# Optimization experiments

Measured on AMD Instinct MI355X. Metric: run time of the kernel, lower is better.

The kernel has to match this reference:

```python
import jax, jax.numpy as jnp
import numpy as np

B, S, D, H = 4, 2048, 1024, 16
DH = D // H


def setup_inputs() -> dict:
    key = jax.random.key(0)
    k1, k2, k3, k4, k5 = jax.random.split(key, 5)
    x = jax.random.normal(k1, (B, S, D), dtype=jnp.float32)
    mask = jnp.tril(jnp.ones((S, S), dtype=bool))  # causal mask
    scale = 1.0 / np.sqrt(D)
    w_qkv = jax.random.normal(k2, (D, 3 * D), dtype=jnp.float32) * scale
    b_qkv = jnp.zeros((3 * D,), dtype=jnp.float32)
    w_out = jax.random.normal(k3, (D, D), dtype=jnp.float32) * scale
    b_out = jnp.zeros((D,), dtype=jnp.float32)
    return {"x": x, "w_qkv": w_qkv, "b_qkv": b_qkv, "w_out": w_out, "b_out": b_out, "mask": mask}


def reference(x, w_qkv, b_qkv, w_out, b_out, mask):
    qkv = jnp.einsum('bsd,de->bse', x, w_qkv) + b_qkv  # (B,S,3D)
    q, k, v = jnp.split(qkv, 3, axis=-1)
    # (B,S,D) -> (B,H,S,DH)
    q = q.reshape(B, S, H, DH).transpose(0, 2, 1, 3)
    k = k.reshape(B, S, H, DH).transpose(0, 2, 1, 3)
    v = v.reshape(B, S, H, DH).transpose(0, 2, 1, 3)
    scores = jnp.einsum('bhqd,bhkd->bhqk', q, k) / jnp.sqrt(jnp.float32(DH))
    scores = jnp.where(mask[None, None, :, :], scores, -jnp.inf)
    attn = jax.nn.softmax(scores, axis=-1)  # dropout p=0.0 -> identity
    out = jnp.einsum('bhqk,bhkd->bhqd', attn, v)
    out = out.transpose(0, 2, 1, 3).reshape(B, S, D)
    return jnp.einsum('bsd,de->bse', out, w_out) + b_out
```

## Files before the change

### kernel.cpp

```cpp
#include <hip/hip_runtime.h>
#include <hip/hip_bf16.h>

typedef unsigned short u16;
typedef __bf16 bf16x8 __attribute__((ext_vector_type(8)));
typedef float f32x4 __attribute__((ext_vector_type(4)));
typedef unsigned short u16x8 __attribute__((ext_vector_type(8)));

__device__ __forceinline__ void async_copy16(void* lds, const void* g) {
  __builtin_amdgcn_global_load_lds(
      (const __attribute__((address_space(1))) unsigned int*)g,
      (__attribute__((address_space(3))) unsigned int*)lds, 16, 0, 0);
}

__device__ __forceinline__ u16 f2bf(float f) {
  __hip_bfloat16 h = __float2bfloat16(f);
  u16 u;
  __builtin_memcpy(&u, &h, 2);
  return u;
}

__device__ __forceinline__ u16 f2bf_rne(float f) {
  unsigned b = __builtin_bit_cast(unsigned, f);
  b += 0x7FFF + ((b >> 16) & 1);
  return (u16)(b >> 16);
}

__device__ __forceinline__ unsigned cvt_pk_bf16(float a, float b) {
  unsigned r;
  asm("v_cvt_pk_bf16_f32 %0, %1, %2" : "=v"(r) : "v"(a), "v"(b));
  return r;
}

__global__ void k_f32_to_bf16(const float* __restrict__ in, u16* __restrict__ out, int n4) {
  int i = blockIdx.x * blockDim.x + threadIdx.x;
  if (i >= n4) return;
  float4 v = ((const float4*)in)[i];
  ushort4 o;
  o.x = f2bf(v.x); o.y = f2bf(v.y); o.z = f2bf(v.z); o.w = f2bf(v.w);
  ((ushort4*)out)[i] = o;
}

__global__ void k_transpose_bf16(const float* __restrict__ in, u16* __restrict__ out, int R, int C) {
  __shared__ float tile[32][33];
  int bx = blockIdx.x * 32;
  int by = blockIdx.y * 32;
  int tx = threadIdx.x & 31, ty = threadIdx.x >> 5;
  for (int i = ty; i < 32; i += 8) tile[i][tx] = in[(size_t)(by + i) * C + bx + tx];
  __syncthreads();
  for (int i = ty; i < 32; i += 8) out[(size_t)(bx + i) * R + by + tx] = f2bf(tile[tx][i]);
}

template <int OUT_BF16>
__global__ __launch_bounds__(256, 2) void k_gemm_bt(
    const u16* __restrict__ A, const u16* __restrict__ Bt,
    const float* __restrict__ bias, void* __restrict__ Cout,
    int M, int N, int K) {
  __shared__ __align__(16) u16 As[128][32];
  __shared__ __align__(16) u16 Bs[128][32];
  const int t = threadIdx.x;
  const int l = t & 63, w = t >> 6;
  const int lr = l & 15, lk = l >> 4;
  const int wr = w >> 1, wc = w & 1;
  const int m0 = blockIdx.x * 128, n0 = blockIdx.y * 128;

  f32x4 acc[4][4] = {};

  for (int k0 = 0; k0 < K; k0 += 32) {
    __syncthreads();
    for (int c = 0; c < 2; ++c) {
      int idx = c * 256 + t;
      int row = idx >> 2, slot = idx & 3;
      int sw = (slot ^ ((row >> 1) & 3)) << 3;
      async_copy16((char*)&As[0][0] + idx * 16, A + (size_t)(m0 + row) * K + k0 + sw);
      async_copy16((char*)&Bs[0][0] + idx * 16, Bt + (size_t)(n0 + row) * K + k0 + sw);
    }
    __syncthreads();
    bf16x8 af[4], bfr[4];
    for (int m = 0; m < 4; ++m) {
      int row = wr * 64 + m * 16 + lr;
      af[m] = *(const bf16x8*)((const char*)&As[0][0] + row * 64 + ((lk ^ ((row >> 1) & 3)) << 4));
    }
    for (int n = 0; n < 4; ++n) {
      int row = wc * 64 + n * 16 + lr;
      bfr[n] = *(const bf16x8*)((const char*)&Bs[0][0] + row * 64 + ((lk ^ ((row >> 1) & 3)) << 4));
    }
    for (int m = 0; m < 4; ++m)
      for (int n = 0; n < 4; ++n)
        acc[m][n] = __builtin_amdgcn_mfma_f32_16x16x32_bf16(af[m], bfr[n], acc[m][n], 0, 0, 0);
  }

  for (int n = 0; n < 4; ++n) {
    int col = n0 + wc * 64 + n * 16 + lr;
    float bv = bias[col];
    for (int m = 0; m < 4; ++m) {
      int rowb = m0 + wr * 64 + m * 16 + lk * 4;
      for (int r = 0; r < 4; ++r) {
        float v = acc[m][n][r] + bv;
        size_t off = (size_t)(rowb + r) * N + col;
        if constexpr (OUT_BF16) ((u16*)Cout)[off] = f2bf(v);
        else ((float*)Cout)[off] = v;
      }
    }
  }
}

__global__ __launch_bounds__(256, 3) void k_attn(
    const u16* __restrict__ QKV,
    u16* __restrict__ O) {
  const int bh = blockIdx.x;
  const int qt = 15 - blockIdx.y;
  const int b = bh >> 4, h = bh & 15;
  const int t = threadIdx.x;
  const int l = t & 63, w = t >> 6;
  const int lr = l & 15, lk = l >> 4;
  constexpr float LG = 0.18033688f;

  __shared__ __align__(16) u16 Ks[2][64][64];
  __shared__ __align__(16) u16 VT[2][64][64];
  __shared__ __align__(16) u16 Pl[4][32][64];

  const u16* Kb0 = QKV + (size_t)b * 2048 * 3072 + 1024 + h * 64;
  const u16* Vb0 = Kb0 + 1024;

  u16x8 vreg[2];

  auto stageK = [&](int j, int buf) {
#pragma unroll
    for (int c = 0; c < 2; ++c) {
      int gi = c * 256 + t;
      int row = gi >> 3, slot = gi & 7;
      async_copy16((char*)&Ks[buf][0][0] + gi * 16,
                   Kb0 + ((size_t)j * 64 + row) * 3072 + ((slot ^ (row & 7)) << 3));
    }
  };
  auto loadV = [&](int j) {
#pragma unroll
    for (int c = 0; c < 2; ++c) {
      int r = c * 32 + (t >> 3), dh0 = (t & 7) << 3;
      vreg[c] = *(const u16x8*)(Vb0 + ((size_t)j * 64 + r) * 3072 + dh0);
    }
  };
  auto writeV = [&](int buf) {
#pragma unroll
    for (int c = 0; c < 2; ++c) {
      int r = c * 32 + (t >> 3), dh0 = (t & 7) << 3;
#pragma unroll
      for (int jj = 0; jj < 8; ++jj) {
        int dh = dh0 + jj;
        int phi = (dh & 7) ^ ((dh >> 3) & 7);
        VT[buf][dh][((((r >> 3) ^ phi) & 7) << 3) | (r & 7)] = vreg[c][jj];
      }
    }
  };

  const int nt = 2 * qt + 2;
  const int q0w = qt * 128 + w * 32;
  const size_t rowQ = (size_t)b * 2048 + q0w;

  bf16x8 qf[2][2];
#pragma unroll
  for (int g = 0; g < 2; ++g)
#pragma unroll
    for (int c = 0; c < 2; ++c)
      qf[g][c] = *(const bf16x8*)(QKV + (rowQ + g * 16 + lr) * 3072 + h * 64 + c * 32 + lk * 8);

  f32x4 acc[2][4] = {};
  float mi[2], li[2];
#pragma unroll
  for (int g = 0; g < 2; ++g) { mi[g] = -__builtin_inff(); li[g] = 0.f; }

  stageK(0, 0);
  loadV(0);
  writeV(0);
  __syncthreads();

  for (int j = 0; j < nt; ++j) {
    const int cur = j & 1;
    const bool more = (j + 1 < nt);
    if (more) { stageK(j + 1, cur ^ 1); loadV(j + 1); }

    f32x4 s[2][4] = {};
    __builtin_amdgcn_s_setprio(1);
#pragma unroll
    for (int c = 0; c < 2; ++c)
#pragma unroll
      for (int n = 0; n < 4; ++n) {
        int row = n * 16 + lr;
        bf16x8 kf = *(const bf16x8*)((const char*)&Ks[cur][0][0] + row * 128 +
                                     ((((c * 4 + lk) ^ (row & 7)) & 7) << 4));
        s[0][n] = __builtin_amdgcn_mfma_f32_16x16x32_bf16(kf, qf[0][c], s[0][n], 0, 0, 0);
        s[1][n] = __builtin_amdgcn_mfma_f32_16x16x32_bf16(kf, qf[1][c], s[1][n], 0, 0, 0);
      }
    __builtin_amdgcn_s_setprio(0);

    if (j * 64 + 63 > q0w) {
      const int kb = j * 64 + lk * 4;
#pragma unroll
      for (int g = 0; g < 2; ++g) {
        const int qq = q0w + g * 16 + lr;
#pragma unroll
        for (int n = 0; n < 4; ++n)
#pragma unroll
          for (int r = 0; r < 4; ++r)
            if (kb + n * 16 + r > qq) s[g][n][r] = -__builtin_inff();
      }
    }

    float tm[2];
#pragma unroll
    for (int g = 0; g < 2; ++g) {
      float m0 = fmaxf(fmaxf(s[g][0][0], s[g][0][1]), fmaxf(s[g][0][2], s[g][0][3]));
      float m1 = fmaxf(fmaxf(s[g][1][0], s[g][1][1]), fmaxf(s[g][1][2], s[g][1][3]));
      float m2 = fmaxf(fmaxf(s[g][2][0], s[g][2][1]), fmaxf(s[g][2][2], s[g][2][3]));
      float m3 = fmaxf(fmaxf(s[g][3][0], s[g][3][1]), fmaxf(s[g][3][2], s[g][3][3]));
      float x = fmaxf(fmaxf(m0, m1), fmaxf(m2, m3));
      x = fmaxf(x, __shfl_xor(x, 16));
      x = fmaxf(x, __shfl_xor(x, 32));
      tm[g] = x;
    }
    if (__any((tm[0] > mi[0] + 64.0f) || (tm[1] > mi[1] + 64.0f))) {
#pragma unroll
      for (int g = 0; g < 2; ++g) {
        float mnew = fmaxf(mi[g], tm[g]);
        float alpha = __builtin_amdgcn_exp2f((mi[g] - mnew) * LG);
        mi[g] = mnew;
        li[g] *= alpha;
        float a0 = __shfl(alpha, lk * 4 + 0);
        float a1 = __shfl(alpha, lk * 4 + 1);
        float a2 = __shfl(alpha, lk * 4 + 2);
        float a3 = __shfl(alpha, lk * 4 + 3);
#pragma unroll
        for (int n = 0; n < 4; ++n) {
          acc[g][n][0] *= a0; acc[g][n][1] *= a1; acc[g][n][2] *= a2; acc[g][n][3] *= a3;
        }
      }
    }

    u16* pw = &Pl[w][0][0];
#pragma unroll
    for (int g = 0; g < 2; ++g) {
      const float mc = -mi[g] * LG;
      float ps = 0.f;
#pragma unroll
      for (int n = 0; n < 4; ++n) {
        float p0 = __builtin_amdgcn_exp2f(fmaf(s[g][n][0], LG, mc));
        float p1 = __builtin_amdgcn_exp2f(fmaf(s[g][n][1], LG, mc));
        float p2 = __builtin_amdgcn_exp2f(fmaf(s[g][n][2], LG, mc));
        float p3 = __builtin_amdgcn_exp2f(fmaf(s[g][n][3], LG, mc));
        ps += (p0 + p1) + (p2 + p3);
        unsigned w0 = cvt_pk_bf16(p0, p1);
        unsigned w1 = cvt_pk_bf16(p2, p3);
        int kc = (n * 2 + (lk >> 1)) ^ (lr & 7);
        *(uint2*)(pw + (g * 16 + lr) * 64 + kc * 8 + (lk & 1) * 4) = make_uint2(w0, w1);
      }
      ps += __shfl_xor(ps, 16);
      ps += __shfl_xor(ps, 32);
      li[g] += ps;
    }

    __builtin_amdgcn_s_setprio(1);
#pragma unroll
    for (int c = 0; c < 2; ++c) {
      bf16x8 pa0 = *(const bf16x8*)(pw + lr * 64 + (((c * 4 + lk) ^ (lr & 7)) << 3));
      bf16x8 pa1 = *(const bf16x8*)(pw + (16 + lr) * 64 + (((c * 4 + lk) ^ (lr & 7)) << 3));
#pragma unroll
      for (int n = 0; n < 4; ++n) {
        int dh = n * 16 + lr;
        int phi = (dh & 7) ^ ((dh >> 3) & 7);
        bf16x8 vf = *(const bf16x8*)((const char*)&VT[cur][0][0] + dh * 128 +
                                     ((((c * 4 + lk) ^ phi) & 7) << 4));
        acc[0][n] = __builtin_amdgcn_mfma_f32_16x16x32_bf16(pa0, vf, acc[0][n], 0, 0, 0);
        acc[1][n] = __builtin_amdgcn_mfma_f32_16x16x32_bf16(pa1, vf, acc[1][n], 0, 0, 0);
      }
    }
    __builtin_amdgcn_s_setprio(0);

    if (more) writeV(cur ^ 1);
    __syncthreads();
  }

#pragma unroll
  for (int g = 0; g < 2; ++g) {
    float l0 = __shfl(li[g], lk * 4 + 0);
    float l1 = __shfl(li[g], lk * 4 + 1);
    float l2 = __shfl(li[g], lk * 4 + 2);
    float l3 = __shfl(li[g], lk * 4 + 3);
    float inv[4] = {1.0f / l0, 1.0f / l1, 1.0f / l2, 1.0f / l3};
#pragma unroll
    for (int r = 0; r < 4; ++r) {
      size_t orow = (rowQ + g * 16 + lk * 4 + r) * 1024 + h * 64;
#pragma unroll
      for (int n = 0; n < 4; ++n) O[orow + n * 16 + lr] = f2bf_rne(acc[g][n][r] * inv[r]);
    }
  }
}

extern "C" void kernel_launch(void* const* d_in, const int* in_sizes, int n_in,
                              void* d_out, int out_size, void* d_ws, size_t ws_size,
                              hipStream_t stream) {
  const float* x = (const float*)d_in[0];
  const float* w_qkv = (const float*)d_in[1];
  const float* b_qkv = (const float*)d_in[2];
  const float* w_out = (const float*)d_in[3];
  const float* b_out = (const float*)d_in[4];

  char* ws = (char*)d_ws;
  u16* X16 = (u16*)(ws);
  u16* WqkvT = (u16*)(ws + 16777216);
  u16* WoutT = (u16*)(ws + 23068672);
  u16* QKVb = (u16*)(ws + 25165824);
  u16* O16 = X16;

  k_f32_to_bf16<<<8192, 256, 0, stream>>>(x, X16, 8388608 / 4);
  k_transpose_bf16<<<dim3(96, 32), 256, 0, stream>>>(w_qkv, WqkvT, 1024, 3072);
  k_transpose_bf16<<<dim3(32, 32), 256, 0, stream>>>(w_out, WoutT, 1024, 1024);
  k_gemm_bt<1><<<dim3(64, 24), 256, 0, stream>>>(X16, WqkvT, b_qkv, QKVb, 8192, 3072, 1024);
  k_attn<<<dim3(64, 16), 256, 0, stream>>>(QKVb, O16);
  k_gemm_bt<0><<<dim3(64, 8), 256, 0, stream>>>(O16, WoutT, b_out, d_out, 8192, 1024, 1024);
}
```

Measured before the change: 175.0 us.

## Triple-buffer GEMM LDS tiles with async prefetch two stages ahead

The GEMM kernel's single LDS tile pair becomes a three-stage ring buffer. Global-to-LDS async copies are issued two k-steps ahead, and completion is gated with explicit vmcnt waits plus a single barrier per iteration, replacing the two syncthreads. The aim is to overlap global load latency with MFMA work. Launch bounds rise to 3 blocks per CU, and the triple buffer triples LDS use to 48KB per block, which could limit occupancy. The hand-written waitcnt and barrier sequence is fragile if the compiler reorders or merges the loads.

```diff
diff --git a/kernel.cpp b/kernel.cpp
--- a/kernel.cpp
+++ b/kernel.cpp
@@ -51,42 +51,63 @@
 }
 
 template <int OUT_BF16>
-__global__ __launch_bounds__(256, 2) void k_gemm_bt(
+__global__ __launch_bounds__(256, 3) void k_gemm_bt(
     const u16* __restrict__ A, const u16* __restrict__ Bt,
     const float* __restrict__ bias, void* __restrict__ Cout,
     int M, int N, int K) {
-  __shared__ __align__(16) u16 As[128][32];
-  __shared__ __align__(16) u16 Bs[128][32];
+  __shared__ __align__(16) u16 As[3][128][32];
+  __shared__ __align__(16) u16 Bs[3][128][32];
   const int t = threadIdx.x;
   const int l = t & 63, w = t >> 6;
   const int lr = l & 15, lk = l >> 4;
   const int wr = w >> 1, wc = w & 1;
   const int m0 = blockIdx.x * 128, n0 = blockIdx.y * 128;
-
-  f32x4 acc[4][4] = {};
-
-  for (int k0 = 0; k0 < K; k0 += 32) {
-    __syncthreads();
+  const int nk = K >> 5;
+
+  auto stage = [&](int kt) {
+    int buf = kt - (kt / 3) * 3;
+    int k0 = kt * 32;
+#pragma unroll
     for (int c = 0; c < 2; ++c) {
       int idx = c * 256 + t;
       int row = idx >> 2, slot = idx & 3;
       int sw = (slot ^ ((row >> 1) & 3)) << 3;
-      async_copy16((char*)&As[0][0] + idx * 16, A + (size_t)(m0 + row) * K + k0 + sw);
-      async_copy16((char*)&Bs[0][0] + idx * 16, Bt + (size_t)(n0 + row) * K + k0 + sw);
-    }
-    __syncthreads();
+      async_copy16((char*)&As[buf][0][0] + idx * 16, A + (size_t)(m0 + row) * K + k0 + sw);
+      async_copy16((char*)&Bs[buf][0][0] + idx * 16, Bt + (size_t)(n0 + row) * K + k0 + sw);
+    }
+  };
+
+  f32x4 acc[4][4] = {};
+
+  stage(0);
+  stage(1);
+  asm volatile("s_waitcnt vmcnt(4)" ::: "memory");
+  asm volatile("s_barrier" ::: "memory");
+
+  for (int kt = 0; kt < nk; ++kt) {
+    const int buf = kt - (kt / 3) * 3;
+    if (kt + 2 < nk) stage(kt + 2);
+
     bf16x8 af[4], bfr[4];
+#pragma unroll
     for (int m = 0; m < 4; ++m) {
       int row = wr * 64 + m * 16 + lr;
-      af[m] = *(const bf16x8*)((const char*)&As[0][0] + row * 64 + ((lk ^ ((row >> 1) & 3)) << 4));
-    }
+      af[m] = *(const bf16x8*)((const char*)&As[buf][0][0] + row * 64 + ((lk ^ ((row >> 1) & 3)) << 4));
+    }
+#pragma unroll
     for (int n = 0; n < 4; ++n) {
       int row = wc * 64 + n * 16 + lr;
-      bfr[n] = *(const bf16x8*)((const char*)&Bs[0][0] + row * 64 + ((lk ^ ((row >> 1) & 3)) << 4));
-    }
+      bfr[n] = *(const bf16x8*)((const char*)&Bs[buf][0][0] + row * 64 + ((lk ^ ((row >> 1) & 3)) << 4));
+    }
+#pragma unroll
     for (int m = 0; m < 4; ++m)
+#pragma unroll
       for (int n = 0; n < 4; ++n)
         acc[m][n] = __builtin_amdgcn_mfma_f32_16x16x32_bf16(af[m], bfr[n], acc[m][n], 0, 0, 0);
+
+    if (kt + 2 < nk) asm volatile("s_waitcnt vmcnt(4)" ::: "memory");
+    else asm volatile("s_waitcnt vmcnt(0)" ::: "memory");
+    asm volatile("s_barrier" ::: "memory");
   }
 
   for (int n = 0; n < 4; ++n) {
```

Result: no change. 175.8 us (+0.5%).
